# Kernel tuning notes

Measured on AMD Instinct MI355X. Metric: run time of the kernel, lower is better.

Reference implementation:

```python
import jax, jax.numpy as jnp
import numpy as np

B, S, D, H, E = 4, 1024, 1024, 16, 4
HD = D // H
EPS = 1e-5


def setup_inputs() -> dict:
    key = jax.random.key(0)
    ks = jax.random.split(key, 6)
    std = 0.02
    return {
        "hidden_states": jax.random.normal(ks[0], (B, S, D), dtype=jnp.float32),
        "Wr": jax.random.normal(ks[1], (D, E), dtype=jnp.float32) * std,
        "br": jnp.zeros((E,), jnp.float32),
        "ln_g": jnp.ones((E, D), jnp.float32),
        "ln_b": jnp.zeros((E, D), jnp.float32),
        "W_attn": jax.random.normal(ks[2], (E, D, 3 * D), dtype=jnp.float32) * std,
        "b_attn": jnp.zeros((E, 3 * D), jnp.float32),
        "W_proj": jax.random.normal(ks[3], (E, D, D), dtype=jnp.float32) * std,
        "b_proj": jnp.zeros((E, D), jnp.float32),
    }


def reference(hidden_states, Wr, br, ln_g, ln_b, W_attn, b_attn, W_proj, b_proj):
    b, s, d = hidden_states.shape
    x = hidden_states.reshape(b * s, d)  # [N, D]

    # naive softmax router over experts
    score = jax.nn.softmax(x @ Wr + br, axis=-1)  # [N, E]

    # LayerNorm stats are expert-independent; affine is per-expert
    mu = jnp.mean(x, axis=-1, keepdims=True)
    var = jnp.mean(jnp.square(x - mu), axis=-1, keepdims=True)
    xn = (x - mu) * jax.lax.rsqrt(var + EPS)  # [N, D]

    ln_out = xn[:, None, :] * ln_g[None] + ln_b[None]  # [N, E, D]
    qkv_all = jnp.einsum('ned,edf->nef', ln_out, W_attn) + b_attn  # [N, E, 3D]
    # weighted_qkv: scale each expert's qkv by its routing score, sum
    qkv = jnp.einsum('ne,nef->nf', score, qkv_all)  # [N, 3D]

    q, k, v = jnp.split(qkv.reshape(b, s, 3 * d), 3, axis=-1)
    def split_heads(t):
        return t.reshape(b, s, H, HD).transpose(0, 2, 1, 3)  # [B,H,S,hd]
    q, k, v = split_heads(q), split_heads(k), split_heads(v)

    scale = 1.0 / jnp.sqrt(jnp.asarray(HD, q.dtype))
    att = jnp.einsum('bhqd,bhkd->bhqk', q, k) * scale  # [B,H,S,S]
    causal = jnp.tril(jnp.ones((s, s), dtype=bool))
    att = jnp.where(causal[None, None], att, jnp.finfo(att.dtype).min)
    probs = jax.nn.softmax(att, axis=-1)
    ctx = jnp.einsum('bhqk,bhkd->bhqd', probs, v)  # [B,H,S,hd]
    ctx = ctx.transpose(0, 2, 1, 3).reshape(b * s, d)  # [N, D]

    proj_all = jnp.einsum('nd,edf->nef', ctx, W_proj) + b_proj  # [N, E, D]
    out = jnp.einsum('ne,nef->nf', score, proj_all).reshape(b, s, d)
    return out
```

## Files before the change

### kernel.cpp

```cpp
#include <hip/hip_runtime.h>
#include <stdint.h>

#define NB 4
#define SS 1024
#define DD 1024
#define EE 4
#define HH 16
#define HDD 64
#define NN (NB*SS)
#define KK2 (EE*DD)
#define FF1 (3*DD)

typedef __attribute__((ext_vector_type(4))) float f32x4;
typedef __attribute__((ext_vector_type(8))) _Float16 half8;
typedef __attribute__((ext_vector_type(4))) _Float16 half4;

static __device__ __forceinline__ f32x4 mfma16(half8 a, half8 b, f32x4 c){
  return __builtin_amdgcn_mfma_f32_16x16x32_f16(a, b, c, 0, 0, 0);
}

#define GLOAD_LDS16(gp, lp) __builtin_amdgcn_global_load_lds( \
    (const unsigned int __attribute__((address_space(1)))*)(uintptr_t)(gp), \
    (unsigned int __attribute__((address_space(3)))*)(uintptr_t)(lp), 16, 0, 0)

#define SBAR() do { asm volatile("" ::: "memory"); \
                    __builtin_amdgcn_s_barrier(); \
                    asm volatile("" ::: "memory"); } while(0)

__global__ __launch_bounds__(256) void prep_kernel(
    const float* __restrict__ x, const float* __restrict__ Wr,
    const float* __restrict__ br, const float* __restrict__ ln_g,
    const float* __restrict__ ln_b, float* __restrict__ score,
    _Float16* __restrict__ A1)
{
  int n = blockIdx.x;
  int tid = threadIdx.x;
  float4 xv = ((const float4*)(x + (size_t)n*DD))[tid];
  float xa[4] = {xv.x, xv.y, xv.z, xv.w};
  float vals[6];
  vals[0] = xa[0]+xa[1]+xa[2]+xa[3];
  vals[1] = xa[0]*xa[0]+xa[1]*xa[1]+xa[2]*xa[2]+xa[3]*xa[3];
  vals[2] = vals[3] = vals[4] = vals[5] = 0.f;
  #pragma unroll
  for (int j = 0; j < 4; ++j){
    float4 w = ((const float4*)Wr)[tid*4 + j];
    vals[2] += xa[j]*w.x; vals[3] += xa[j]*w.y;
    vals[4] += xa[j]*w.z; vals[5] += xa[j]*w.w;
  }
  #pragma unroll
  for (int off = 32; off >= 1; off >>= 1)
    #pragma unroll
    for (int i = 0; i < 6; ++i)
      vals[i] += __shfl_xor(vals[i], off, 64);
  __shared__ float red[4][6];
  int wid = tid >> 6;
  if ((tid & 63) == 0){
    #pragma unroll
    for (int i = 0; i < 6; ++i) red[wid][i] = vals[i];
  }
  __syncthreads();
  float tot[6];
  #pragma unroll
  for (int i = 0; i < 6; ++i)
    tot[i] = red[0][i] + red[1][i] + red[2][i] + red[3][i];

  float mu   = tot[0] * (1.f/DD);
  float var  = tot[1] * (1.f/DD) - mu*mu;
  float rsig = rsqrtf(var + 1e-5f);
  float lg[4];
  #pragma unroll
  for (int e = 0; e < 4; ++e) lg[e] = tot[2+e] + br[e];
  float mx = fmaxf(fmaxf(lg[0], lg[1]), fmaxf(lg[2], lg[3]));
  float ex[4], esum = 0.f;
  #pragma unroll
  for (int e = 0; e < 4; ++e){ ex[e] = __expf(lg[e] - mx); esum += ex[e]; }
  float sc[4];
  #pragma unroll
  for (int e = 0; e < 4; ++e) sc[e] = ex[e] / esum;
  if (tid < 4) score[n*4 + tid] = sc[tid];

  float xn[4];
  #pragma unroll
  for (int j = 0; j < 4; ++j) xn[j] = (xa[j] - mu) * rsig;
  int d0 = tid*4;
  #pragma unroll
  for (int e = 0; e < 4; ++e){
    float4 gg = ((const float4*)(ln_g + e*DD))[tid];
    float4 bb = ((const float4*)(ln_b + e*DD))[tid];
    half4 o;
    o[0] = (_Float16)(sc[e]*(xn[0]*gg.x + bb.x));
    o[1] = (_Float16)(sc[e]*(xn[1]*gg.y + bb.y));
    o[2] = (_Float16)(sc[e]*(xn[2]*gg.z + bb.z));
    o[3] = (_Float16)(sc[e]*(xn[3]*gg.w + bb.w));
    *(half4*)(A1 + (size_t)n*KK2 + e*DD + d0) = o;
  }
}

__global__ __launch_bounds__(256) void transpose_f16_kernel(
    const float* __restrict__ W, _Float16* __restrict__ WT, int K, int F)
{
  __shared__ float t[64][65];
  int k0 = blockIdx.x * 64, f0 = blockIdx.y * 64;
  int tid = threadIdx.x;
  int r = tid >> 4, c4 = (tid & 15) * 4;
  #pragma unroll
  for (int i = 0; i < 4; ++i){
    float4 v = *(const float4*)(W + (size_t)(k0 + i*16 + r)*F + f0 + c4);
    t[i*16 + r][c4+0] = v.x; t[i*16 + r][c4+1] = v.y;
    t[i*16 + r][c4+2] = v.z; t[i*16 + r][c4+3] = v.w;
  }
  __syncthreads();
  int f = tid >> 2, seg = tid & 3;
  half8 o0, o1;
  #pragma unroll
  for (int j = 0; j < 8; ++j){
    o0[j] = (_Float16)t[seg*16 + j][f];
    o1[j] = (_Float16)t[seg*16 + 8 + j][f];
  }
  _Float16* dst = WT + (size_t)(f0 + f)*K + k0 + seg*16;
  *(half8*)dst = o0;
  *(half8*)(dst + 8) = o1;
}

#define G1_BM 256
#define G1_BN 192
#define G1_BK 64
#define G1_T  (KK2/G1_BK)
#define G1_ABUF (G1_BM*G1_BK)
#define G1_BBUF (G1_BN*G1_BK)
#define G1_BUFSZ (G1_ABUF+G1_BBUF)

__global__ __launch_bounds__(512, 2) void gemm1_kernel(
    const _Float16* __restrict__ A, const _Float16* __restrict__ BT,
    const float* __restrict__ score, const float* __restrict__ bias,
    _Float16* __restrict__ C)
{
  __shared__ _Float16 smem[2*G1_BUFSZ];
  int tid = threadIdx.x;
  int lane = tid & 63, wid = tid >> 6;
  int q = lane & 15, g = lane >> 4;
  int wr = wid >> 1, wc = wid & 1;
  int xo = (q & 7) << 3;
  int bid = blockIdx.x;
  int xcd = bid & 7, li = bid >> 3;
  int m0 = (li >> 1) * G1_BM;
  int n0 = (xcd*2 + (li & 1)) * G1_BN;

  int arow[4], brow[6];
  #pragma unroll
  for (int mf = 0; mf < 4; ++mf) arow[mf] = (wr*64 + mf*16 + q)*64;
  #pragma unroll
  for (int nf = 0; nf < 6; ++nf) brow[nf] = G1_ABUF + (wc*96 + nf*16 + q)*64;
  int soff[2] = { (g*8) ^ xo, (32 + g*8) ^ xo };

  auto stageA = [&](int t, int buf, int h){
    const int k0 = t * G1_BK;
    _Float16* sA = smem + buf*G1_BUFSZ;
    #pragma unroll
    for (int ld = 0; ld < 2; ++ld){
      int l = h*2 + ld;
      int c = l*512 + tid;
      int row = c >> 3;
      int seg = (c & 7) ^ (row & 7);
      GLOAD_LDS16(A + (size_t)(m0 + row)*KK2 + k0 + seg*8,
                  sA + (l*512 + wid*64)*8);
    }
  };
  auto stageB = [&](int t, int buf){
    const int k0 = t * G1_BK;
    _Float16* sB = smem + buf*G1_BUFSZ + G1_ABUF;
    #pragma unroll
    for (int ld = 0; ld < 3; ++ld){
      int c = ld*512 + tid;
      int row = c >> 3;
      int seg = (c & 7) ^ (row & 7);
      GLOAD_LDS16(BT + (size_t)(n0 + row)*KK2 + k0 + seg*8,
                  sB + (ld*512 + wid*64)*8);
    }
  };

  f32x4 acc[4][6] = {};
  half8 af0[2][2], af2[2][2], bf[6][2];

  stageA(0, 0, 0); stageA(0, 0, 1); stageB(0, 0);

  for (int t = 0; t < G1_T-1; ++t){
    int buf = t & 1, nxt = buf ^ 1;
    const _Float16* base = smem + buf*G1_BUFSZ;
    stageA(t+1, nxt, 0);
    asm volatile("s_waitcnt vmcnt(2)" ::: "memory");
    SBAR();
    #pragma unroll
    for (int m = 0; m < 2; ++m)
      #pragma unroll
      for (int k = 0; k < 2; ++k)
        af0[m][k] = *(const half8*)(base + arow[m] + soff[k]);
    #pragma unroll
    for (int n = 0; n < 3; ++n)
      #pragma unroll
      for (int k = 0; k < 2; ++k)
        bf[n][k] = *(const half8*)(base + brow[n] + soff[k]);
    stageA(t+1, nxt, 1);
    __builtin_amdgcn_s_setprio(1);
    #pragma unroll
    for (int k = 0; k < 2; ++k)
      #pragma unroll
      for (int m = 0; m < 2; ++m)
        #pragma unroll
        for (int n = 0; n < 3; ++n)
          acc[m][n] = mfma16(af0[m][k], bf[n][k], acc[m][n]);
    __builtin_amdgcn_s_setprio(0);
    SBAR();
    #pragma unroll
    for (int n = 3; n < 6; ++n)
      #pragma unroll
      for (int k = 0; k < 2; ++k)
        bf[n][k] = *(const half8*)(base + brow[n] + soff[k]);
    stageB(t+1, nxt);
    __builtin_amdgcn_s_setprio(1);
    #pragma unroll
    for (int k = 0; k < 2; ++k)
      #pragma unroll
      for (int m = 0; m < 2; ++m)
        #pragma unroll
        for (int n = 3; n < 6; ++n)
          acc[m][n] = mfma16(af0[m][k], bf[n][k], acc[m][n]);
    __builtin_amdgcn_s_setprio(0);
    SBAR();
    #pragma unroll
    for (int m = 0; m < 2; ++m)
      #pragma unroll
      for (int k = 0; k < 2; ++k)
        af2[m][k] = *(const half8*)(base + arow[2+m] + soff[k]);
    __builtin_amdgcn_s_setprio(1);
    #pragma unroll
    for (int k = 0; k < 2; ++k)
      #pragma unroll
      for (int m = 0; m < 2; ++m)
        #pragma unroll
        for (int n = 3; n < 6; ++n)
          acc[2+m][n] = mfma16(af2[m][k], bf[n][k], acc[2+m][n]);
    __builtin_amdgcn_s_setprio(0);
    SBAR();
    __builtin_amdgcn_s_setprio(1);
    #pragma unroll
    for (int k = 0; k < 2; ++k)
      #pragma unroll
      for (int m = 0; m < 2; ++m)
        #pragma unroll
        for (int n = 0; n < 3; ++n)
          acc[2+m][n] = mfma16(af2[m][k], bf[n][k], acc[2+m][n]);
    __builtin_amdgcn_s_setprio(0);
  }
  {
    const _Float16* base = smem + ((G1_T-1) & 1)*G1_BUFSZ;
    asm volatile("s_waitcnt vmcnt(0)" ::: "memory");
    SBAR();
    #pragma unroll
    for (int m = 0; m < 2; ++m)
      #pragma unroll
      for (int k = 0; k < 2; ++k){
        af0[m][k] = *(const half8*)(base + arow[m] + soff[k]);
        af2[m][k] = *(const half8*)(base + arow[2+m] + soff[k]);
      }
    #pragma unroll
    for (int n = 0; n < 6; ++n)
      #pragma unroll
      for (int k = 0; k < 2; ++k)
        bf[n][k] = *(const half8*)(base + brow[n] + soff[k]);
    #pragma unroll
    for (int k = 0; k < 2; ++k)
      #pragma unroll
      for (int m = 0; m < 2; ++m)
        #pragma unroll
        for (int n = 0; n < 6; ++n){
          acc[m][n]   = mfma16(af0[m][k], bf[n][k], acc[m][n]);
          acc[2+m][n] = mfma16(af2[m][k], bf[n][k], acc[2+m][n]);
        }
  }

  float bv[6][4];
  #pragma unroll
  for (int nf = 0; nf < 6; ++nf){
    int gn = n0 + wc*96 + nf*16 + q;
    #pragma unroll
    for (int e = 0; e < 4; ++e) bv[nf][e] = bias[e*FF1 + gn];
  }
  #pragma unroll
  for (int mf = 0; mf < 4; ++mf){
    #pragma unroll
    for (int r = 0; r < 4; ++r){
      int gm = m0 + wr*64 + mf*16 + g*4 + r;
      float4 sc = *(const float4*)(score + gm*4);
      #pragma unroll
      for (int nf = 0; nf < 6; ++nf){
        int gn = n0 + wc*96 + nf*16 + q;
        float v = acc[mf][nf][r]
                + sc.x*bv[nf][0] + sc.y*bv[nf][1] + sc.z*bv[nf][2] + sc.w*bv[nf][3];
        C[(size_t)gm*FF1 + gn] = (_Float16)v;
      }
    }
  }
}

#define G2_BK 64
#define G2_ABUF (128*G2_BK)
#define G2_BUFSZ (2*G2_ABUF)

__global__ __launch_bounds__(512) void gemm2_kernel(
    const _Float16* __restrict__ A, const _Float16* __restrict__ BT,
    const float* __restrict__ score, const float* __restrict__ bias,
    float* __restrict__ Cout)
{
  __shared__ _Float16 smem[2*G2_BUFSZ];
  int tid = threadIdx.x;
  int lane = tid & 63, wid = tid >> 6;
  int q = lane & 15, g = lane >> 4;
  int wr = wid >> 2, wc = wid & 3;
  int xo = (q & 7) << 3;
  int bid = blockIdx.x;
  int xcd = bid >> 5, idx = bid & 31;
  int m0 = (xcd*4 + (idx >> 3)) * 128;
  int n0 = (idx & 7) * 128;

  int arow[4], brow[2];
  #pragma unroll
  for (int mf = 0; mf < 4; ++mf) arow[mf] = (wr*64 + mf*16 + q)*64;
  #pragma unroll
  for (int nf = 0; nf < 2; ++nf) brow[nf] = G2_ABUF + (wc*32 + nf*16 + q)*64;
  int soff[2] = { (g*8) ^ xo, (32 + g*8) ^ xo };

  auto stage = [&](int t, int buf){
    const int k0 = t * G2_BK;
    _Float16* sA = smem + buf*G2_BUFSZ;
    _Float16* sB = sA + G2_ABUF;
    #pragma unroll
    for (int ld = 0; ld < 2; ++ld){
      int c = ld*512 + tid;
      int row = c >> 3;
      int seg = (c & 7) ^ (row & 7);
      GLOAD_LDS16(A + (size_t)(m0 + row)*KK2 + k0 + seg*8,
                  sA + (ld*512 + wid*64)*8);
    }
    #pragma unroll
    for (int ld = 0; ld < 2; ++ld){
      int c = ld*512 + tid;
      int row = c >> 3;
      int seg = (c & 7) ^ (row & 7);
      GLOAD_LDS16(BT + (size_t)(n0 + row)*KK2 + k0 + seg*8,
                  sB + (ld*512 + wid*64)*8);
    }
  };

  f32x4 acc[4][2] = {};

  auto compute = [&](int buf){
    const _Float16* base = smem + buf*G2_BUFSZ;
    half8 af[4][2], bfr[2][2];
    #pragma unroll
    for (int m = 0; m < 4; ++m)
      #pragma unroll
      for (int k = 0; k < 2; ++k)
        af[m][k] = *(const half8*)(base + arow[m] + soff[k]);
    #pragma unroll
    for (int n = 0; n < 2; ++n)
      #pragma unroll
      for (int k = 0; k < 2; ++k)
        bfr[n][k] = *(const half8*)(base + brow[n] + soff[k]);
    __builtin_amdgcn_s_setprio(1);
    #pragma unroll
    for (int k = 0; k < 2; ++k)
      #pragma unroll
      for (int m = 0; m < 4; ++m)
        #pragma unroll
        for (int n = 0; n < 2; ++n)
          acc[m][n] = mfma16(af[m][k], bfr[n][k], acc[m][n]);
    __builtin_amdgcn_s_setprio(0);
  };

  stage(0, 0);
  for (int t = 0; t < KK2/G2_BK - 1; ++t){
    stage(t+1, (t+1)&1);
    asm volatile("s_waitcnt vmcnt(4)" ::: "memory");
    SBAR();
    compute(t & 1);
    SBAR();
  }
  asm volatile("s_waitcnt vmcnt(0)" ::: "memory");
  SBAR();
  compute((KK2/G2_BK - 1) & 1);

  #pragma unroll
  for (int m = 0; m < 4; ++m){
    #pragma unroll
    for (int r = 0; r < 4; ++r){
      int gm = m0 + wr*64 + m*16 + g*4 + r;
      float4 sc = *(const float4*)(score + gm*4);
      #pragma unroll
      for (int n = 0; n < 2; ++n){
        int gn = n0 + wc*32 + n*16 + q;
        float v = acc[m][n][r]
                + sc.x*bias[gn] + sc.y*bias[DD+gn]
                + sc.z*bias[2*DD+gn] + sc.w*bias[3*DD+gn];
        Cout[(size_t)gm*DD + gn] = v;
      }
    }
  }
}

__global__ __launch_bounds__(256) void attn_kernel(
    const _Float16* __restrict__ qkv, _Float16* __restrict__ ctx)
{
  __shared__ _Float16 lsK[64*64];
  __shared__ _Float16 lsV[64*64];
  __shared__ _Float16 lsP[4][16*64];
  int bh = blockIdx.x, qt = blockIdx.y;
  int b = bh >> 4, h = bh & 15;
  int tid = threadIdx.x, lane = tid & 63, wid = tid >> 6;
  int q = lane & 15, g = lane >> 4;
  int xo = (q & 7) << 3;
  int qrow0 = qt*64 + wid*16;

  half8 qf[2];
  #pragma unroll
  for (int kk = 0; kk < 2; ++kk)
    qf[kk] = *(const half8*)(qkv + ((size_t)b*SS + qrow0 + q)*FF1 + h*HDD + kk*32 + g*8);

  f32x4 o[4] = {};
  float mrow = -1e30f, lsum = 0.f;
  const float SC2 = 0.18033688011112042f;
  int qglob = qrow0 + q;

  for (int kt = 0; kt <= qt; ++kt){
    __syncthreads();
    size_t kvrow = (size_t)b*SS + kt*64;
    #pragma unroll
    for (int i = 0; i < 2; ++i){
      int c = i*256 + tid;
      int row = c >> 3, seg = (c & 7) ^ (row & 7);
      GLOAD_LDS16(qkv + (kvrow + row)*FF1 + DD + h*HDD + seg*8,
                  lsK + (size_t)(i*256 + wid*64)*8);
    }
    #pragma unroll
    for (int i = 0; i < 2; ++i){
      int p = wid*2 + i;
      half8 v = *(const half8*)(qkv + (kvrow + lane)*FF1 + 2*DD + h*HDD + p*8);
      #pragma unroll
      for (int j = 0; j < 8; ++j){
        int hd = p*8 + j;
        lsV[hd*64 + (lane ^ ((hd & 7) << 3))] = v[j];
      }
    }
    __syncthreads();

    f32x4 st[4] = {};
    #pragma unroll
    for (int i = 0; i < 4; ++i){
      #pragma unroll
      for (int kk = 0; kk < 2; ++kk){
        half8 kf = *(const half8*)(lsK + (i*16 + q)*64 + ((kk*32 + g*8) ^ xo));
        st[i] = mfma16(kf, qf[kk], st[i]);
      }
    }
    float pvv[16]; float tm = -1e30f;
    #pragma unroll
    for (int i = 0; i < 4; ++i)
      #pragma unroll
      for (int r = 0; r < 4; ++r){
        int kglob = kt*64 + i*16 + g*4 + r;
        float sv = (kglob <= qglob) ? st[i][r]*SC2 : -1e30f;
        pvv[i*4+r] = sv; tm = fmaxf(tm, sv);
      }
    tm = fmaxf(tm, __shfl_xor(tm, 16, 64));
    tm = fmaxf(tm, __shfl_xor(tm, 32, 64));
    float mnew  = fmaxf(mrow, tm);
    float alpha = exp2f(mrow - mnew);
    mrow = mnew;
    float psum = 0.f;
    _Float16 pb[16];
    #pragma unroll
    for (int i = 0; i < 16; ++i){
      float p = exp2f(pvv[i] - mnew);
      psum += p; pb[i] = (_Float16)p;
    }
    lsum = lsum*alpha + psum;
    float af4[4];
    #pragma unroll
    for (int r = 0; r < 4; ++r) af4[r] = __shfl(alpha, g*4 + r, 64);
    #pragma unroll
    for (int n = 0; n < 4; ++n)
      #pragma unroll
      for (int r = 0; r < 4; ++r) o[n][r] *= af4[r];
    #pragma unroll
    for (int i = 0; i < 4; ++i){
      half4 w4;
      w4[0]=pb[i*4+0]; w4[1]=pb[i*4+1]; w4[2]=pb[i*4+2]; w4[3]=pb[i*4+3];
      *(half4*)(&lsP[wid][q*64 + ((i*16 + g*4) ^ xo)]) = w4;
    }
    #pragma unroll
    for (int kk = 0; kk < 2; ++kk){
      half8 pf = *(const half8*)(&lsP[wid][q*64 + ((kk*32 + g*8) ^ xo)]);
      #pragma unroll
      for (int n = 0; n < 4; ++n){
        half8 vf = *(const half8*)(&lsV[(n*16 + q)*64 + ((kk*32 + g*8) ^ xo)]);
        o[n] = mfma16(pf, vf, o[n]);
      }
    }
  }
  float lt = lsum + __shfl_xor(lsum, 16, 64);
  lt = lt + __shfl_xor(lt, 32, 64);
  float rinv = 1.f / lt;
  #pragma unroll
  for (int r = 0; r < 4; ++r){
    float ri = __shfl(rinv, g*4 + r, 64);
    int qg = qt*64 + wid*16 + g*4 + r;
    _Float16* obase = ctx + ((size_t)b*SS + qg)*DD + h*HDD;
    #pragma unroll
    for (int n = 0; n < 4; ++n)
      obase[n*16 + q] = (_Float16)(o[n][r] * ri);
  }
}

__global__ __launch_bounds__(256) void expand_kernel(
    const _Float16* __restrict__ ctx, const float* __restrict__ score,
    _Float16* __restrict__ A2)
{
  int idx = blockIdx.x*256 + threadIdx.x;
  int n = idx >> 7, s8 = idx & 127;
  half8 v = *(const half8*)(ctx + (size_t)n*DD + s8*8);
  float4 sc = *(const float4*)(score + n*4);
  float f[8];
  #pragma unroll
  for (int j = 0; j < 8; ++j) f[j] = (float)v[j];
  float scs[4] = {sc.x, sc.y, sc.z, sc.w};
  #pragma unroll
  for (int e = 0; e < 4; ++e){
    half8 o;
    #pragma unroll
    for (int j = 0; j < 8; ++j) o[j] = (_Float16)(f[j]*scs[e]);
    *(half8*)(A2 + (size_t)n*KK2 + e*DD + s8*8) = o;
  }
}

extern "C" void kernel_launch(void* const* d_in, const int* in_sizes, int n_in,
                              void* d_out, int out_size, void* d_ws, size_t ws_size,
                              hipStream_t stream)
{
  const float* x      = (const float*)d_in[0];
  const float* Wr     = (const float*)d_in[1];
  const float* br     = (const float*)d_in[2];
  const float* ln_g   = (const float*)d_in[3];
  const float* ln_b   = (const float*)d_in[4];
  const float* W_attn = (const float*)d_in[5];
  const float* b_attn = (const float*)d_in[6];
  const float* W_proj = (const float*)d_in[7];
  const float* b_proj = (const float*)d_in[8];
  (void)in_sizes; (void)n_in; (void)out_size; (void)ws_size;

  char* ws = (char*)d_ws;
  size_t off = 0;
  auto alloc = [&](size_t bytes) -> void* {
    void* p = ws + off; off += (bytes + 255) & ~(size_t)255; return p;
  };
  _Float16* W1T   = (_Float16*)alloc((size_t)FF1*KK2*2);
  _Float16* W2T   = (_Float16*)alloc((size_t)DD*KK2*2);
  float*    score = (float*)   alloc((size_t)NN*4*4);
  _Float16* A1    = (_Float16*)alloc((size_t)NN*KK2*2);
  _Float16* qkv   = (_Float16*)alloc((size_t)NN*FF1*2);
  _Float16* ctx   = (_Float16*)alloc((size_t)NN*DD*2);

  hipLaunchKernelGGL(transpose_f16_kernel, dim3(KK2/64, FF1/64), dim3(256), 0, stream,
                     W_attn, W1T, KK2, FF1);
  hipLaunchKernelGGL(transpose_f16_kernel, dim3(KK2/64, DD/64), dim3(256), 0, stream,
                     W_proj, W2T, KK2, DD);
  hipLaunchKernelGGL(prep_kernel, dim3(NN), dim3(256), 0, stream,
                     x, Wr, br, ln_g, ln_b, score, A1);
  hipLaunchKernelGGL(gemm1_kernel, dim3(256), dim3(512), 0, stream,
                     A1, W1T, score, b_attn, qkv);
  hipLaunchKernelGGL(attn_kernel, dim3(NB*HH, SS/64), dim3(256), 0, stream,
                     qkv, ctx);
  hipLaunchKernelGGL(expand_kernel, dim3(NN*128/256), dim3(256), 0, stream,
                     ctx, score, A1);
  hipLaunchKernelGGL(gemm2_kernel, dim3(256), dim3(512), 0, stream,
                     A1, W2T, score, b_proj, (float*)d_out);
}
```

Baseline: 212.9 us.

## Fold LayerNorm affine into weights and apply routing scores inside GEMMs

The LayerNorm gain is folded into the transposed W_attn and the bias term b·W is precomputed into a per-expert bias. The GEMMs now read the expert-independent normalized input and ctx, which are 4x smaller than the materialized A operands. In GEMM1 the per-row score is applied to the A fragments in fp16 before each MFMA; in GEMM2 the score is applied to fp32 partial accumulators at each expert boundary. This removes the expand kernel and the large A1/A2 writes and reads, at the cost of extra vector multiplies in the GEMM inner loop, fp16 score rounding, and an extra bias-reduction kernel.

```diff
diff --git a/kernel.cpp b/kernel.cpp
--- a/kernel.cpp
+++ b/kernel.cpp
@@ -29,9 +29,8 @@
 
 __global__ __launch_bounds__(256) void prep_kernel(
     const float* __restrict__ x, const float* __restrict__ Wr,
-    const float* __restrict__ br, const float* __restrict__ ln_g,
-    const float* __restrict__ ln_b, float* __restrict__ score,
-    _Float16* __restrict__ A1)
+    const float* __restrict__ br, float* __restrict__ score,
+    _Float16* __restrict__ xnb)
 {
   int n = blockIdx.x;
   int tid = threadIdx.x;
@@ -74,40 +73,42 @@
   float ex[4], esum = 0.f;
   #pragma unroll
   for (int e = 0; e < 4; ++e){ ex[e] = __expf(lg[e] - mx); esum += ex[e]; }
-  float sc[4];
-  #pragma unroll
-  for (int e = 0; e < 4; ++e) sc[e] = ex[e] / esum;
-  if (tid < 4) score[n*4 + tid] = sc[tid];
-
-  float xn[4];
-  #pragma unroll
-  for (int j = 0; j < 4; ++j) xn[j] = (xa[j] - mu) * rsig;
-  int d0 = tid*4;
-  #pragma unroll
-  for (int e = 0; e < 4; ++e){
-    float4 gg = ((const float4*)(ln_g + e*DD))[tid];
-    float4 bb = ((const float4*)(ln_b + e*DD))[tid];
-    half4 o;
-    o[0] = (_Float16)(sc[e]*(xn[0]*gg.x + bb.x));
-    o[1] = (_Float16)(sc[e]*(xn[1]*gg.y + bb.y));
-    o[2] = (_Float16)(sc[e]*(xn[2]*gg.z + bb.z));
-    o[3] = (_Float16)(sc[e]*(xn[3]*gg.w + bb.w));
-    *(half4*)(A1 + (size_t)n*KK2 + e*DD + d0) = o;
-  }
-}
-
+  if (tid < 4) score[n*4 + tid] = ex[tid] / esum;
+
+  half4 o;
+  #pragma unroll
+  for (int j = 0; j < 4; ++j) o[j] = (_Float16)((xa[j] - mu) * rsig);
+  *(half4*)(xnb + (size_t)n*DD + tid*4) = o;
+}
+
+template<bool AFFINE>
 __global__ __launch_bounds__(256) void transpose_f16_kernel(
-    const float* __restrict__ W, _Float16* __restrict__ WT, int K, int F)
+    const float* __restrict__ W, _Float16* __restrict__ WT, int K, int F,
+    const float* __restrict__ gvec, const float* __restrict__ bvec,
+    float* __restrict__ part)
 {
   __shared__ float t[64][65];
+  __shared__ float red2[16][64];
   int k0 = blockIdx.x * 64, f0 = blockIdx.y * 64;
   int tid = threadIdx.x;
   int r = tid >> 4, c4 = (tid & 15) * 4;
+  float pf[4] = {0.f, 0.f, 0.f, 0.f};
   #pragma unroll
   for (int i = 0; i < 4; ++i){
-    float4 v = *(const float4*)(W + (size_t)(k0 + i*16 + r)*F + f0 + c4);
+    int k = k0 + i*16 + r;
+    float4 v = *(const float4*)(W + (size_t)k*F + f0 + c4);
+    if constexpr (AFFINE){
+      float bk = bvec[k];
+      pf[0] += bk*v.x; pf[1] += bk*v.y; pf[2] += bk*v.z; pf[3] += bk*v.w;
+      float gk = gvec[k];
+      v.x *= gk; v.y *= gk; v.z *= gk; v.w *= gk;
+    }
     t[i*16 + r][c4+0] = v.x; t[i*16 + r][c4+1] = v.y;
     t[i*16 + r][c4+2] = v.z; t[i*16 + r][c4+3] = v.w;
+  }
+  if constexpr (AFFINE){
+    #pragma unroll
+    for (int j = 0; j < 4; ++j) red2[r][c4+j] = pf[j];
   }
   __syncthreads();
   int f = tid >> 2, seg = tid & 3;
@@ -120,6 +121,27 @@
   _Float16* dst = WT + (size_t)(f0 + f)*K + k0 + seg*16;
   *(half8*)dst = o0;
   *(half8*)(dst + 8) = o1;
+  if constexpr (AFFINE){
+    if (tid < 64){
+      float s = 0.f;
+      #pragma unroll
+      for (int rr = 0; rr < 16; ++rr) s += red2[rr][tid];
+      part[(size_t)blockIdx.x * F + f0 + tid] = s;
+    }
+  }
+}
+
+__global__ __launch_bounds__(256) void bb1_kernel(
+    const float* __restrict__ b_attn, const float* __restrict__ part,
+    float* __restrict__ BB1)
+{
+  int idx = blockIdx.x*256 + threadIdx.x;
+  int e = idx / FF1, f = idx - e*FF1;
+  float s = b_attn[idx];
+  #pragma unroll
+  for (int i = 0; i < 16; ++i)
+    s += part[(size_t)(e*16 + i)*FF1 + f];
+  BB1[idx] = s;
 }
 
 #define G1_BM 256
@@ -131,7 +153,7 @@
 #define G1_BUFSZ (G1_ABUF+G1_BBUF)
 
 __global__ __launch_bounds__(512, 2) void gemm1_kernel(
-    const _Float16* __restrict__ A, const _Float16* __restrict__ BT,
+    const _Float16* __restrict__ XN, const _Float16* __restrict__ BT,
     const float* __restrict__ score, const float* __restrict__ bias,
     _Float16* __restrict__ C)
 {
@@ -154,7 +176,7 @@
   int soff[2] = { (g*8) ^ xo, (32 + g*8) ^ xo };
 
   auto stageA = [&](int t, int buf, int h){
-    const int k0 = t * G1_BK;
+    const int d0 = (t & 15) * G1_BK;
     _Float16* sA = smem + buf*G1_BUFSZ;
     #pragma unroll
     for (int ld = 0; ld < 2; ++ld){
@@ -162,7 +184,7 @@
       int c = l*512 + tid;
       int row = c >> 3;
       int seg = (c & 7) ^ (row & 7);
-      GLOAD_LDS16(A + (size_t)(m0 + row)*KK2 + k0 + seg*8,
+      GLOAD_LDS16(XN + (size_t)(m0 + row)*DD + d0 + seg*8,
                   sA + (l*512 + wid*64)*8);
     }
   };
@@ -181,10 +203,24 @@
 
   f32x4 acc[4][6] = {};
   half8 af0[2][2], af2[2][2], bf[6][2];
+  _Float16 sc16[4];
+
+  auto scale8 = [](half8 v, _Float16 s){
+    half8 r;
+    #pragma unroll
+    for (int j = 0; j < 8; ++j) r[j] = v[j]*s;
+    return r;
+  };
 
   stageA(0, 0, 0); stageA(0, 0, 1); stageB(0, 0);
 
   for (int t = 0; t < G1_T-1; ++t){
+    if ((t & 15) == 0){
+      int e = t >> 4;
+      #pragma unroll
+      for (int mf = 0; mf < 4; ++mf)
+        sc16[mf] = (_Float16)score[(size_t)(m0 + wr*64 + mf*16 + q)*4 + e];
+    }
     int buf = t & 1, nxt = buf ^ 1;
     const _Float16* base = smem + buf*G1_BUFSZ;
     stageA(t+1, nxt, 0);
@@ -194,7 +230,7 @@
     for (int m = 0; m < 2; ++m)
       #pragma unroll
       for (int k = 0; k < 2; ++k)
-        af0[m][k] = *(const half8*)(base + arow[m] + soff[k]);
+        af0[m][k] = scale8(*(const half8*)(base + arow[m] + soff[k]), sc16[m]);
     #pragma unroll
     for (int n = 0; n < 3; ++n)
       #pragma unroll
@@ -231,7 +267,7 @@
     for (int m = 0; m < 2; ++m)
       #pragma unroll
       for (int k = 0; k < 2; ++k)
-        af2[m][k] = *(const half8*)(base + arow[2+m] + soff[k]);
+        af2[m][k] = scale8(*(const half8*)(base + arow[2+m] + soff[k]), sc16[2+m]);
     __builtin_amdgcn_s_setprio(1);
     #pragma unroll
     for (int k = 0; k < 2; ++k)
@@ -260,8 +296,8 @@
     for (int m = 0; m < 2; ++m)
       #pragma unroll
       for (int k = 0; k < 2; ++k){
-        af0[m][k] = *(const half8*)(base + arow[m] + soff[k]);
-        af2[m][k] = *(const half8*)(base + arow[2+m] + soff[k]);
+        af0[m][k] = scale8(*(const half8*)(base + arow[m] + soff[k]), sc16[m]);
+        af2[m][k] = scale8(*(const half8*)(base + arow[2+m] + soff[k]), sc16[2+m]);
       }
     #pragma unroll
     for (int n = 0; n < 6; ++n)
@@ -308,7 +344,7 @@
 #define G2_BUFSZ (2*G2_ABUF)
 
 __global__ __launch_bounds__(512) void gemm2_kernel(
-    const _Float16* __restrict__ A, const _Float16* __restrict__ BT,
+    const _Float16* __restrict__ CTX, const _Float16* __restrict__ BT,
     const float* __restrict__ score, const float* __restrict__ bias,
     float* __restrict__ Cout)
 {
@@ -331,6 +367,7 @@
   int soff[2] = { (g*8) ^ xo, (32 + g*8) ^ xo };
 
   auto stage = [&](int t, int buf){
+    const int d0 = (t & 15) * G2_BK;
     const int k0 = t * G2_BK;
     _Float16* sA = smem + buf*G2_BUFSZ;
     _Float16* sB = sA + G2_ABUF;
@@ -339,7 +376,7 @@
       int c = ld*512 + tid;
       int row = c >> 3;
       int seg = (c & 7) ^ (row & 7);
-      GLOAD_LDS16(A + (size_t)(m0 + row)*KK2 + k0 + seg*8,
+      GLOAD_LDS16(CTX + (size_t)(m0 + row)*DD + d0 + seg*8,
                   sA + (ld*512 + wid*64)*8);
     }
     #pragma unroll
@@ -352,7 +389,7 @@
     }
   };
 
-  f32x4 acc[4][2] = {};
+  f32x4 accp[4][2] = {}, acco[4][2] = {};
 
   auto compute = [&](int buf){
     const _Float16* base = smem + buf*G2_BUFSZ;
@@ -374,8 +411,23 @@
       for (int m = 0; m < 4; ++m)
         #pragma unroll
         for (int n = 0; n < 2; ++n)
-          acc[m][n] = mfma16(af[m][k], bfr[n][k], acc[m][n]);
+          accp[m][n] = mfma16(af[m][k], bfr[n][k], accp[m][n]);
     __builtin_amdgcn_s_setprio(0);
+  };
+
+  auto merge = [&](int e){
+    #pragma unroll
+    for (int m = 0; m < 4; ++m)
+      #pragma unroll
+      for (int r = 0; r < 4; ++r){
+        int gm = m0 + wr*64 + m*16 + g*4 + r;
+        float s = score[(size_t)gm*4 + e];
+        #pragma unroll
+        for (int n = 0; n < 2; ++n){
+          acco[m][n][r] += s*accp[m][n][r];
+          accp[m][n][r] = 0.f;
+        }
+      }
   };
 
   stage(0, 0);
@@ -385,10 +437,12 @@
     SBAR();
     compute(t & 1);
     SBAR();
+    if ((t & 15) == 15) merge(t >> 4);
   }
   asm volatile("s_waitcnt vmcnt(0)" ::: "memory");
   SBAR();
   compute((KK2/G2_BK - 1) & 1);
+  merge(3);
 
   #pragma unroll
   for (int m = 0; m < 4; ++m){
@@ -399,7 +453,7 @@
       #pragma unroll
       for (int n = 0; n < 2; ++n){
         int gn = n0 + wc*32 + n*16 + q;
-        float v = acc[m][n][r]
+        float v = acco[m][n][r]
                 + sc.x*bias[gn] + sc.y*bias[DD+gn]
                 + sc.z*bias[2*DD+gn] + sc.w*bias[3*DD+gn];
         Cout[(size_t)gm*DD + gn] = v;
@@ -518,27 +572,6 @@
     #pragma unroll
     for (int n = 0; n < 4; ++n)
       obase[n*16 + q] = (_Float16)(o[n][r] * ri);
-  }
-}
-
-__global__ __launch_bounds__(256) void expand_kernel(
-    const _Float16* __restrict__ ctx, const float* __restrict__ score,
-    _Float16* __restrict__ A2)
-{
-  int idx = blockIdx.x*256 + threadIdx.x;
-  int n = idx >> 7, s8 = idx & 127;
-  half8 v = *(const half8*)(ctx + (size_t)n*DD + s8*8);
-  float4 sc = *(const float4*)(score + n*4);
-  float f[8];
-  #pragma unroll
-  for (int j = 0; j < 8; ++j) f[j] = (float)v[j];
-  float scs[4] = {sc.x, sc.y, sc.z, sc.w};
-  #pragma unroll
-  for (int e = 0; e < 4; ++e){
-    half8 o;
-    #pragma unroll
-    for (int j = 0; j < 8; ++j) o[j] = (_Float16)(f[j]*scs[e]);
-    *(half8*)(A2 + (size_t)n*KK2 + e*DD + s8*8) = o;
   }
 }
 
@@ -562,25 +595,27 @@
   auto alloc = [&](size_t bytes) -> void* {
     void* p = ws + off; off += (bytes + 255) & ~(size_t)255; return p;
   };
-  _Float16* W1T   = (_Float16*)alloc((size_t)FF1*KK2*2);
+  _Float16* W1gT  = (_Float16*)alloc((size_t)FF1*KK2*2);
   _Float16* W2T   = (_Float16*)alloc((size_t)DD*KK2*2);
   float*    score = (float*)   alloc((size_t)NN*4*4);
-  _Float16* A1    = (_Float16*)alloc((size_t)NN*KK2*2);
+  _Float16* xn16  = (_Float16*)alloc((size_t)NN*DD*2);
   _Float16* qkv   = (_Float16*)alloc((size_t)NN*FF1*2);
   _Float16* ctx   = (_Float16*)alloc((size_t)NN*DD*2);
-
-  hipLaunchKernelGGL(transpose_f16_kernel, dim3(KK2/64, FF1/64), dim3(256), 0, stream,
-                     W_attn, W1T, KK2, FF1);
-  hipLaunchKernelGGL(transpose_f16_kernel, dim3(KK2/64, DD/64), dim3(256), 0, stream,
-                     W_proj, W2T, KK2, DD);
+  float*    part  = (float*)   alloc((size_t)(KK2/64)*FF1*4);
+  float*    BB1   = (float*)   alloc((size_t)EE*FF1*4);
+
+  hipLaunchKernelGGL((transpose_f16_kernel<true>), dim3(KK2/64, FF1/64), dim3(256), 0, stream,
+                     W_attn, W1gT, KK2, FF1, ln_g, ln_b, part);
+  hipLaunchKernelGGL((transpose_f16_kernel<false>), dim3(KK2/64, DD/64), dim3(256), 0, stream,
+                     W_proj, W2T, KK2, DD, nullptr, nullptr, nullptr);
+  hipLaunchKernelGGL(bb1_kernel, dim3(EE*FF1/256), dim3(256), 0, stream,
+                     b_attn, part, BB1);
   hipLaunchKernelGGL(prep_kernel, dim3(NN), dim3(256), 0, stream,
-                     x, Wr, br, ln_g, ln_b, score, A1);
+                     x, Wr, br, score, xn16);
   hipLaunchKernelGGL(gemm1_kernel, dim3(256), dim3(512), 0, stream,
-                     A1, W1T, score, b_attn, qkv);
+                     xn16, W1gT, score, BB1, qkv);
   hipLaunchKernelGGL(attn_kernel, dim3(NB*HH, SS/64), dim3(256), 0, stream,
                      qkv, ctx);
-  hipLaunchKernelGGL(expand_kernel, dim3(NN*128/256), dim3(256), 0, stream,
-                     ctx, score, A1);
   hipLaunchKernelGGL(gemm2_kernel, dim3(256), dim3(512), 0, stream,
-                     A1, W2T, score, b_proj, (float*)d_out);
-}
+                     ctx, W2T, score, b_proj, (float*)d_out);
+}
```

Result: no change. 212.5 us (-0.2%).
